# Kernel optimization log

Hardware: AMD Instinct MI355X
Metric: run time of the kernel (lower is better)

Reference implementation:

```python
import jax, jax.numpy as jnp
import numpy as np

N, E, F, L, G, T = 50000, 800000, 128, 3, 256, 10


def _lin_init(key, shape, fan_in):
    s = 1.0 / np.sqrt(fan_in)
    return jax.random.uniform(key, shape, jnp.float32, -s, s)


def setup_inputs() -> dict:
    key = jax.random.key(0)
    ks = jax.random.split(key, 10)
    x = jax.random.normal(ks[0], (N, F), jnp.float32)
    edge_index = jax.random.randint(ks[1], (2, E), 0, N, jnp.int64)
    batch = jnp.sort(jax.random.randint(ks[2], (N,), 0, G, jnp.int64))
    Wl = _lin_init(ks[3], (L, F, F), F)   # lin_l weight per layer
    bl = _lin_init(ks[4], (L, F), F)      # lin_l bias per layer
    Wr = _lin_init(ks[5], (L, F, F), F)   # lin_r weight per layer (no bias)
    W1 = _lin_init(ks[6], (F, L * F), L * F)
    b1 = _lin_init(ks[7], (F,), L * F)
    W2 = _lin_init(ks[8], (T, F), F)
    b2 = _lin_init(ks[9], (T,), F)
    return {"x": x, "edge_index": edge_index, "batch": batch, "Wl": Wl,
            "bl": bl, "Wr": Wr, "W1": W1, "b1": b1, "W2": W2, "b2": b2}


def reference(x, edge_index, batch, Wl, bl, Wr, W1, b1, W2, b2):
    src, dst = edge_index[0], edge_index[1]
    n = x.shape[0]
    # in-degree for mean aggregation (zero-degree nodes -> 0, like scatter_mean)
    deg = jax.ops.segment_sum(jnp.ones_like(src, dtype=x.dtype), dst, num_segments=n)
    inv_deg = jnp.where(deg > 0, 1.0 / deg, 0.0)[:, None]
    h = x
    feats = []
    for i in range(L):
        # SAGEConv (aggr='mean'): out = lin_l(mean_j x_j) + lin_r(x_i)
        agg = jax.ops.segment_sum(h[src], dst, num_segments=n) * inv_deg
        h = agg @ Wl[i].T + bl[i] + h @ Wr[i].T
        feats.append(h)
    hc = jnp.concatenate(feats, axis=1)            # [N, L*F]
    pooled = jax.ops.segment_max(hc, batch, num_segments=G)  # global_max_pool
    z = jax.nn.relu(pooled @ W1.T + b1)
    return z @ W2.T + b2                            # [G, T]
```

## Files before the change

### kernel.cpp

```cpp
#include <hip/hip_runtime.h>
#include <math.h>


typedef __attribute__((ext_vector_type(8))) short short8v;
typedef __attribute__((ext_vector_type(4))) float f32x4;

__device__ __forceinline__ unsigned short bf_hi_bits(float f) {
    union { float f; unsigned u; } c; c.f = f;
    return (unsigned short)(c.u >> 16);
}
__device__ __forceinline__ float bf_to_f(unsigned short h) {
    union { unsigned u; float f; } c; c.u = ((unsigned)h) << 16;
    return c.f;
}
__device__ __forceinline__ unsigned short f2bf_rne(float f) {
    union { float f; unsigned u; } c; c.f = f;
    unsigned u = c.u;
    u += 0x7FFF + ((u >> 16) & 1);
    return (unsigned short)(u >> 16);
}

__global__ void zero_ints(int* __restrict__ p, int n) {
    int i = blockIdx.x * 256 + threadIdx.x;
    if (i < n) p[i] = 0;
}

__global__ void count_deg(const int* __restrict__ dst, int* __restrict__ deg, int E) {
    int e = blockIdx.x * 256 + threadIdx.x;
    if (e < E) atomicAdd(&deg[dst[e]], 1);
}

__global__ __launch_bounds__(256) void block_reduce_deg(const int* __restrict__ deg,
                                                        int* __restrict__ bsum,
                                                        float* __restrict__ inv_deg, int n) {
    __shared__ int s[256];
    int t = threadIdx.x;
    int i = blockIdx.x * 256 + t;
    int d = 0;
    if (i < n) {
        d = deg[i];
        inv_deg[i] = d > 0 ? 1.0f / (float)d : 0.0f;
    }
    s[t] = d;
    __syncthreads();
#pragma unroll
    for (int off = 128; off > 0; off >>= 1) {
        if (t < off) s[t] += s[t + off];
        __syncthreads();
    }
    if (t == 0) bsum[blockIdx.x] = s[0];
}

__global__ __launch_bounds__(256) void scan_bsums(const int* __restrict__ bsum,
                                                  int* __restrict__ boff,
                                                  int* __restrict__ row_ptr, int nb, int n) {
    __shared__ int s[256];
    int t = threadIdx.x;
    int v = (t < nb) ? bsum[t] : 0;
    s[t] = v;
    __syncthreads();
#pragma unroll
    for (int off = 1; off < 256; off <<= 1) {
        int u = (t >= off) ? s[t - off] : 0;
        __syncthreads();
        s[t] += u;
        __syncthreads();
    }
    if (t < nb) boff[t] = s[t] - v;
    if (t == 255) row_ptr[n] = s[255];
}

__global__ __launch_bounds__(256) void scan_fill(const int* __restrict__ deg,
                                                 const int* __restrict__ boff,
                                                 int* __restrict__ row_ptr,
                                                 int* __restrict__ fill_pos, int n) {
    __shared__ int s[256];
    int t = threadIdx.x;
    int i = blockIdx.x * 256 + t;
    int v = (i < n) ? deg[i] : 0;
    s[t] = v;
    __syncthreads();
#pragma unroll
    for (int off = 1; off < 256; off <<= 1) {
        int u = (t >= off) ? s[t - off] : 0;
        __syncthreads();
        s[t] += u;
        __syncthreads();
    }
    if (i < n) {
        int ex = boff[blockIdx.x] + s[t] - v;
        row_ptr[i] = ex;
        fill_pos[i] = ex;
    }
}

__global__ void fill_csr(const int* __restrict__ src, const int* __restrict__ dst,
                         int* __restrict__ fill_pos, int* __restrict__ csr_src, int E) {
    int e = blockIdx.x * 256 + threadIdx.x;
    if (e < E) {
        int d = dst[e];
        int pos = atomicAdd(&fill_pos[d], 1);
        csr_src[pos] = src[e];
    }
}

__global__ void f32_to_bf16(const float* __restrict__ in, unsigned short* __restrict__ out,
                            int n4) {
    int i = blockIdx.x * 256 + threadIdx.x;
    if (i < n4) {
        float4 v = *(const float4*)(in + (size_t)i * 4);
        ushort4 o = {f2bf_rne(v.x), f2bf_rne(v.y), f2bf_rne(v.z), f2bf_rne(v.w)};
        *(ushort4*)(out + (size_t)i * 4) = o;
    }
}

__global__ __launch_bounds__(256) void aggregate_bf(const unsigned short* __restrict__ hb,
                                                    const int* __restrict__ row_ptr,
                                                    const int* __restrict__ csr_src,
                                                    const float* __restrict__ inv_deg,
                                                    float* __restrict__ agg, int n) {
    int node = blockIdx.x * 4 + (threadIdx.x >> 6);
    if (node >= n) return;
    int lane = threadIdx.x & 63;
    int half = lane >> 5;
    int li = lane & 31;
    int j0 = row_ptr[node], j1 = row_ptr[node + 1];
    float a0 = 0.f, a1 = 0.f, a2 = 0.f, a3 = 0.f;
    float b0 = 0.f, b1 = 0.f, b2 = 0.f, b3 = 0.f;
    int j = j0 + half;
    for (; j + 2 < j1; j += 4) {
        int s0 = csr_src[j];
        int s1 = csr_src[j + 2];
        ushort4 v0 = *(const ushort4*)(hb + (size_t)s0 * 128 + li * 4);
        ushort4 v1 = *(const ushort4*)(hb + (size_t)s1 * 128 + li * 4);
        a0 += bf_to_f(v0.x); a1 += bf_to_f(v0.y); a2 += bf_to_f(v0.z); a3 += bf_to_f(v0.w);
        b0 += bf_to_f(v1.x); b1 += bf_to_f(v1.y); b2 += bf_to_f(v1.z); b3 += bf_to_f(v1.w);
    }
    if (j < j1) {
        int s0 = csr_src[j];
        ushort4 v0 = *(const ushort4*)(hb + (size_t)s0 * 128 + li * 4);
        a0 += bf_to_f(v0.x); a1 += bf_to_f(v0.y); a2 += bf_to_f(v0.z); a3 += bf_to_f(v0.w);
    }
    float ax = a0 + b0, ay = a1 + b1, az = a2 + b2, aw = a3 + b3;
    ax += __shfl_xor(ax, 32);
    ay += __shfl_xor(ay, 32);
    az += __shfl_xor(az, 32);
    aw += __shfl_xor(aw, 32);
    if (half == 0) {
        float w = inv_deg[node];
        float4 o = {ax * w, ay * w, az * w, aw * w};
        *(float4*)(agg + (size_t)node * 128 + li * 4) = o;
    }
}

__global__ void prep_wext(const float* __restrict__ Wl, const float* __restrict__ Wr,
                          unsigned short* __restrict__ wext) {
    int idx = blockIdx.x * 256 + threadIdx.x;
    if (idx >= 36864) return;
    int layer = idx / 12288;
    int rem = idx - layer * 12288;
    int s = rem / 2048;
    int rem2 = rem - s * 2048;
    int c = rem2 >> 4;
    int kc = (rem2 & 15) * 8;
    const float* W = (s < 3 ? Wl : Wr) + (size_t)layer * 16384 + c * 128 + kc;
    bool lo = (s % 3) == 1;
    unsigned short* o = wext + (((size_t)layer * 6 + s) * 16384) + c * 128 + kc;
#pragma unroll
    for (int i = 0; i < 8; ++i) {
        float f = W[i];
        unsigned short hb = bf_hi_bits(f);
        if (lo) hb = bf_hi_bits(f - bf_to_f(hb));
        o[i] = hb;
    }
}

__global__ __launch_bounds__(256, 2) void gemm_mfma(const float* __restrict__ A1,
                                                    const float* __restrict__ A2, int stride2,
                                                    const unsigned short* __restrict__ wext,
                                                    const float* __restrict__ bl,
                                                    float* __restrict__ out,
                                                    unsigned short* __restrict__ outb, int n) {
    __shared__ unsigned short Ald[16384];
    __shared__ unsigned short Wld[16384];

    const int tid = threadIdx.x;
    const int row0 = blockIdx.x * 128;
    const int wid = tid >> 6;
    const int lane = tid & 63;
    const int lrow = lane & 15;
    const int lk = lane >> 4;
    const int RowB = (wid >> 1) * 64;
    const int ColB = (wid & 1) * 64;

    const f32x4 zf = {0.f, 0.f, 0.f, 0.f};
    f32x4 acc[4][4];
#pragma unroll
    for (int i = 0; i < 4; ++i)
#pragma unroll
        for (int j = 0; j < 4; ++j) acc[i][j] = zf;

    const int sr = tid >> 1;
    const int sh = tid & 1;
    int grow = row0 + sr;
    if (grow > n - 1) grow = n - 1;
    const float* a1p = A1 + (size_t)grow * 128 + sh * 64;
    const float* a2p = A2 + (size_t)grow * stride2 + sh * 64;
    const int sbyte = sr * 256 + sh * 128;
    const int sswz = (sr & 7) << 4;

    const int needA[6] = {1, 0, 1, 1, 0, 1};
    const int srcA[6] = {0, 0, 0, 1, 1, 1};
    const int loA[6] = {0, 0, 1, 0, 0, 1};

#pragma unroll
    for (int s = 0; s < 6; ++s) {
        const unsigned short* wsrc = wext + s * 16384 + sr * 128 + sh * 64;
#pragma unroll
        for (int i = 0; i < 8; ++i) {
            short8v w = *(const short8v*)(wsrc + i * 8);
            *(short8v*)((char*)Wld + sbyte + ((i * 16) ^ sswz)) = w;
        }
        if (needA[s]) {
            const float* ap = srcA[s] ? a2p : a1p;
            const bool lo = loA[s] != 0;
#pragma unroll
            for (int i = 0; i < 8; ++i) {
                float4 f0 = *(const float4*)(ap + i * 8);
                float4 f1 = *(const float4*)(ap + i * 8 + 4);
                float ff[8] = {f0.x, f0.y, f0.z, f0.w, f1.x, f1.y, f1.z, f1.w};
                short8v v;
#pragma unroll
                for (int j = 0; j < 8; ++j) {
                    unsigned short hb = bf_hi_bits(ff[j]);
                    if (lo) hb = bf_hi_bits(ff[j] - bf_to_f(hb));
                    v[j] = (short)hb;
                }
                *(short8v*)((char*)Ald + sbyte + ((i * 16) ^ sswz)) = v;
            }
        }
        __syncthreads();
#pragma unroll
        for (int ks = 0; ks < 4; ++ks) {
            short8v af[4], bfr[4];
#pragma unroll
            for (int mr = 0; mr < 4; ++mr) {
                int r = RowB + mr * 16 + lrow;
                int byte = (r * 256 + ks * 64 + lk * 16) ^ ((r & 7) << 4);
                af[mr] = *(const short8v*)((const char*)Ald + byte);
            }
#pragma unroll
            for (int nr = 0; nr < 4; ++nr) {
                int c = ColB + nr * 16 + lrow;
                int byte = (c * 256 + ks * 64 + lk * 16) ^ ((c & 7) << 4);
                bfr[nr] = *(const short8v*)((const char*)Wld + byte);
            }
#pragma unroll
            for (int mr = 0; mr < 4; ++mr)
#pragma unroll
                for (int nr = 0; nr < 4; ++nr)
                    acc[mr][nr] = __builtin_amdgcn_mfma_f32_16x16x32_bf16(
                        af[mr], bfr[nr], acc[mr][nr], 0, 0, 0);
        }
        __syncthreads();
    }

#pragma unroll
    for (int nr = 0; nr < 4; ++nr) {
        int col = ColB + nr * 16 + lrow;
        float bias = bl[col];
#pragma unroll
        for (int mr = 0; mr < 4; ++mr) {
            int rbase = row0 + RowB + mr * 16 + lk * 4;
#pragma unroll
            for (int r = 0; r < 4; ++r) {
                int row = rbase + r;
                if (row < n) {
                    float v = acc[mr][nr][r] + bias;
                    out[(size_t)row * 384 + col] = v;
                    if (outb) outb[(size_t)row * 128 + col] = f2bf_rne(v);
                }
            }
        }
    }
}

__global__ void find_starts(const int* __restrict__ batch, int* __restrict__ start, int n, int G) {
    int i = blockIdx.x * 256 + threadIdx.x;
    if (i >= n) return;
    int b = batch[i];
    if (i == 0) {
        for (int g = 0; g <= b; ++g) start[g] = 0;
    } else {
        int pb = batch[i - 1];
        for (int g = pb + 1; g <= b; ++g) start[g] = i;
    }
    if (i == n - 1) {
        for (int g = b + 1; g <= G; ++g) start[g] = n;
    }
}

__global__ __launch_bounds__(384) void pool_max(const float* __restrict__ hc,
                                                const int* __restrict__ start,
                                                float* __restrict__ pooled, int G) {
    int g = blockIdx.x;
    int f = threadIdx.x;
    int s = start[g], e = start[g + 1];
    float m = -INFINITY;
    for (int node = s; node < e; ++node) m = fmaxf(m, hc[(size_t)node * 384 + f]);
    pooled[(size_t)g * 384 + f] = m;
}

__global__ __launch_bounds__(128) void mlp_head(const float* __restrict__ pooled,
                                                const float* __restrict__ W1,
                                                const float* __restrict__ b1,
                                                const float* __restrict__ W2,
                                                const float* __restrict__ b2,
                                                float* __restrict__ out) {
    __shared__ float p[384];
    __shared__ float z[128];
    int g = blockIdx.x, t = threadIdx.x;
    for (int k = t; k < 384; k += 128) p[k] = pooled[(size_t)g * 384 + k];
    __syncthreads();
    float acc = b1[t];
#pragma unroll 4
    for (int k = 0; k < 384; k += 4) {
        float4 w = *(const float4*)(W1 + (size_t)t * 384 + k);
        acc += p[k] * w.x + p[k + 1] * w.y + p[k + 2] * w.z + p[k + 3] * w.w;
    }
    z[t] = fmaxf(acc, 0.f);
    __syncthreads();
    if (t < 10) {
        float a2 = b2[t];
#pragma unroll 8
        for (int k = 0; k < 128; ++k) a2 += z[k] * W2[t * 128 + k];
        out[g * 10 + t] = a2;
    }
}

extern "C" void kernel_launch(void* const* d_in, const int* in_sizes, int n_in,
                              void* d_out, int out_size, void* d_ws, size_t ws_size,
                              hipStream_t stream) {
    const float* x = (const float*)d_in[0];
    const int* edge = (const int*)d_in[1];
    const int* batch = (const int*)d_in[2];
    const float* Wl = (const float*)d_in[3];
    const float* bl = (const float*)d_in[4];
    const float* Wr = (const float*)d_in[5];
    const float* W1 = (const float*)d_in[6];
    const float* b1 = (const float*)d_in[7];
    const float* W2 = (const float*)d_in[8];
    const float* b2 = (const float*)d_in[9];
    float* out = (float*)d_out;

    const int F = 128, G = 256;
    const int N = in_sizes[0] / F;
    const int E = in_sizes[1] / 2;
    const int NB = (N + 255) / 256;

    const int* src = edge;
    const int* dst = edge + E;

    char* p = (char*)d_ws;
    auto alloc = [&](size_t bytes) {
        char* r = p;
        p += (bytes + 15) & ~(size_t)15;
        return r;
    };
    float* hc = (float*)alloc((size_t)N * 384 * 4);
    float* agg = (float*)alloc((size_t)N * 128 * 4);
    float* inv = (float*)alloc((size_t)N * 4);
    float* pooled = (float*)alloc((size_t)G * 384 * 4);
    int* deg = (int*)alloc((size_t)N * 4);
    int* row_ptr = (int*)alloc((size_t)(N + 1) * 4);
    int* fillp = (int*)alloc((size_t)N * 4);
    int* csr = (int*)alloc((size_t)E * 4);
    int* start = (int*)alloc((size_t)(G + 1) * 4);
    unsigned short* wext = (unsigned short*)alloc((size_t)3 * 6 * 16384 * 2);
    int* bsum = (int*)alloc((size_t)NB * 4);
    int* boff = (int*)alloc((size_t)NB * 4);
    unsigned short* hb = (unsigned short*)alloc((size_t)N * 128 * 2);

    zero_ints<<<NB, 256, 0, stream>>>(deg, N);
    count_deg<<<(E + 255) / 256, 256, 0, stream>>>(dst, deg, E);
    block_reduce_deg<<<NB, 256, 0, stream>>>(deg, bsum, inv, N);
    scan_bsums<<<1, 256, 0, stream>>>(bsum, boff, row_ptr, NB, N);
    scan_fill<<<NB, 256, 0, stream>>>(deg, boff, row_ptr, fillp, N);
    fill_csr<<<(E + 255) / 256, 256, 0, stream>>>(src, dst, fillp, csr, E);
    prep_wext<<<144, 256, 0, stream>>>(Wl, Wr, wext);
    f32_to_bf16<<<(N * 32 + 255) / 256, 256, 0, stream>>>(x, hb, N * 32);

    for (int l = 0; l < 3; ++l) {
        const float* hin = (l == 0) ? x : (hc + (size_t)(l - 1) * 128);
        int hstride = (l == 0) ? 128 : 384;
        aggregate_bf<<<(N + 3) / 4, 256, 0, stream>>>(hb, row_ptr, csr, inv, agg, N);
        gemm_mfma<<<(N + 127) / 128, 256, 0, stream>>>(
            agg, hin, hstride, wext + (size_t)l * 6 * 16384, bl + (size_t)l * F,
            hc + (size_t)l * 128, (l < 2) ? hb : (unsigned short*)nullptr, N);
    }

    find_starts<<<NB, 256, 0, stream>>>(batch, start, N, G);
    pool_max<<<G, 384, 0, stream>>>(hc, start, pooled, G);
    mlp_head<<<G, 128, 0, stream>>>(pooled, W1, b1, W2, b2, out);
}
```

Baseline: 500.2 us.

## Store activations as bf16 hi/lo pairs and shrink GEMM row tile to 64

Activations are stored as bf16 hi/lo split pairs instead of fp32. The aggregation kernel now emits the aggregate already split, and the GEMM writes bf16 hi into the concatenated feature buffer plus a lo residual for the next layer. The GEMM loads pre-split bf16 tiles directly, which removes the per-tile fp32-to-bf16 conversion and halves activation traffic. Its row tile shrinks from 128 to 64 with launch bounds raised to 3, giving more blocks and occupancy. The cost is that the pooled features are now bf16-rounded instead of fp32, and each GEMM block has less reuse of the weight tile.

```diff
diff --git a/kernel.cpp b/kernel.cpp
--- a/kernel.cpp
+++ b/kernel.cpp
@@ -104,21 +104,26 @@
     }
 }
 
-__global__ void f32_to_bf16(const float* __restrict__ in, unsigned short* __restrict__ out,
-                            int n4) {
+__global__ void f32_split_bf16(const float* __restrict__ in, unsigned short* __restrict__ hi,
+                               unsigned short* __restrict__ lo, int n4) {
     int i = blockIdx.x * 256 + threadIdx.x;
     if (i < n4) {
         float4 v = *(const float4*)(in + (size_t)i * 4);
-        ushort4 o = {f2bf_rne(v.x), f2bf_rne(v.y), f2bf_rne(v.z), f2bf_rne(v.w)};
-        *(ushort4*)(out + (size_t)i * 4) = o;
+        ushort4 h = {f2bf_rne(v.x), f2bf_rne(v.y), f2bf_rne(v.z), f2bf_rne(v.w)};
+        ushort4 l = {f2bf_rne(v.x - bf_to_f(h.x)), f2bf_rne(v.y - bf_to_f(h.y)),
+                     f2bf_rne(v.z - bf_to_f(h.z)), f2bf_rne(v.w - bf_to_f(h.w))};
+        *(ushort4*)(hi + (size_t)i * 4) = h;
+        *(ushort4*)(lo + (size_t)i * 4) = l;
     }
 }
 
 __global__ __launch_bounds__(256) void aggregate_bf(const unsigned short* __restrict__ hb,
+                                                    int hstride,
                                                     const int* __restrict__ row_ptr,
                                                     const int* __restrict__ csr_src,
                                                     const float* __restrict__ inv_deg,
-                                                    float* __restrict__ agg, int n) {
+                                                    unsigned short* __restrict__ a1hi,
+                                                    unsigned short* __restrict__ a1lo, int n) {
     int node = blockIdx.x * 4 + (threadIdx.x >> 6);
     if (node >= n) return;
     int lane = threadIdx.x & 63;
@@ -131,14 +136,14 @@
     for (; j + 2 < j1; j += 4) {
         int s0 = csr_src[j];
         int s1 = csr_src[j + 2];
-        ushort4 v0 = *(const ushort4*)(hb + (size_t)s0 * 128 + li * 4);
-        ushort4 v1 = *(const ushort4*)(hb + (size_t)s1 * 128 + li * 4);
+        ushort4 v0 = *(const ushort4*)(hb + (size_t)s0 * hstride + li * 4);
+        ushort4 v1 = *(const ushort4*)(hb + (size_t)s1 * hstride + li * 4);
         a0 += bf_to_f(v0.x); a1 += bf_to_f(v0.y); a2 += bf_to_f(v0.z); a3 += bf_to_f(v0.w);
         b0 += bf_to_f(v1.x); b1 += bf_to_f(v1.y); b2 += bf_to_f(v1.z); b3 += bf_to_f(v1.w);
     }
     if (j < j1) {
         int s0 = csr_src[j];
-        ushort4 v0 = *(const ushort4*)(hb + (size_t)s0 * 128 + li * 4);
+        ushort4 v0 = *(const ushort4*)(hb + (size_t)s0 * hstride + li * 4);
         a0 += bf_to_f(v0.x); a1 += bf_to_f(v0.y); a2 += bf_to_f(v0.z); a3 += bf_to_f(v0.w);
     }
     float ax = a0 + b0, ay = a1 + b1, az = a2 + b2, aw = a3 + b3;
@@ -148,8 +153,12 @@
     aw += __shfl_xor(aw, 32);
     if (half == 0) {
         float w = inv_deg[node];
-        float4 o = {ax * w, ay * w, az * w, aw * w};
-        *(float4*)(agg + (size_t)node * 128 + li * 4) = o;
+        float vx = ax * w, vy = ay * w, vz = az * w, vw = aw * w;
+        ushort4 h = {f2bf_rne(vx), f2bf_rne(vy), f2bf_rne(vz), f2bf_rne(vw)};
+        ushort4 l = {f2bf_rne(vx - bf_to_f(h.x)), f2bf_rne(vy - bf_to_f(h.y)),
+                     f2bf_rne(vz - bf_to_f(h.z)), f2bf_rne(vw - bf_to_f(h.w))};
+        *(ushort4*)(a1hi + (size_t)node * 128 + li * 4) = h;
+        *(ushort4*)(a1lo + (size_t)node * 128 + li * 4) = l;
     }
 }
 
@@ -175,82 +184,76 @@
     }
 }
 
-__global__ __launch_bounds__(256, 2) void gemm_mfma(const float* __restrict__ A1,
-                                                    const float* __restrict__ A2, int stride2,
+__global__ __launch_bounds__(256, 3) void gemm_mfma(const unsigned short* __restrict__ a1hi,
+                                                    const unsigned short* __restrict__ a1lo,
+                                                    const unsigned short* __restrict__ a2hi,
+                                                    int stride2,
+                                                    const unsigned short* __restrict__ a2lo,
                                                     const unsigned short* __restrict__ wext,
                                                     const float* __restrict__ bl,
-                                                    float* __restrict__ out,
-                                                    unsigned short* __restrict__ outb, int n) {
-    __shared__ unsigned short Ald[16384];
+                                                    unsigned short* __restrict__ outh,
+                                                    unsigned short* __restrict__ outlo, int n) {
+    __shared__ unsigned short Ald[8192];
     __shared__ unsigned short Wld[16384];
 
     const int tid = threadIdx.x;
-    const int row0 = blockIdx.x * 128;
+    const int row0 = blockIdx.x * 64;
     const int wid = tid >> 6;
     const int lane = tid & 63;
     const int lrow = lane & 15;
     const int lk = lane >> 4;
-    const int RowB = (wid >> 1) * 64;
-    const int ColB = (wid & 1) * 64;
+    const int ColB = wid * 32;
 
     const f32x4 zf = {0.f, 0.f, 0.f, 0.f};
-    f32x4 acc[4][4];
+    f32x4 acc[4][2];
 #pragma unroll
     for (int i = 0; i < 4; ++i)
 #pragma unroll
-        for (int j = 0; j < 4; ++j) acc[i][j] = zf;
-
-    const int sr = tid >> 1;
+        for (int j = 0; j < 2; ++j) acc[i][j] = zf;
+
+    const int sr_a = tid >> 2;
+    const int qa = tid & 3;
+    int growA = row0 + sr_a;
+    if (growA > n - 1) growA = n - 1;
+    const unsigned short* pa1hi = a1hi + (size_t)growA * 128 + qa * 32;
+    const unsigned short* pa1lo = a1lo + (size_t)growA * 128 + qa * 32;
+    const unsigned short* pa2hi = a2hi + (size_t)growA * stride2 + qa * 32;
+    const unsigned short* pa2lo = a2lo + (size_t)growA * 128 + qa * 32;
+    const int aswz = (sr_a & 7) << 4;
+
+    const int sw = tid >> 1;
     const int sh = tid & 1;
-    int grow = row0 + sr;
-    if (grow > n - 1) grow = n - 1;
-    const float* a1p = A1 + (size_t)grow * 128 + sh * 64;
-    const float* a2p = A2 + (size_t)grow * stride2 + sh * 64;
-    const int sbyte = sr * 256 + sh * 128;
-    const int sswz = (sr & 7) << 4;
-
-    const int needA[6] = {1, 0, 1, 1, 0, 1};
-    const int srcA[6] = {0, 0, 0, 1, 1, 1};
-    const int loA[6] = {0, 0, 1, 0, 0, 1};
+    const int wswz = (sw & 7) << 4;
+
+    const unsigned short* asrc[6] = {pa1hi, nullptr, pa1lo, pa2hi, nullptr, pa2lo};
 
 #pragma unroll
     for (int s = 0; s < 6; ++s) {
-        const unsigned short* wsrc = wext + s * 16384 + sr * 128 + sh * 64;
+        const unsigned short* wsrc = wext + s * 16384 + sw * 128 + sh * 64;
 #pragma unroll
         for (int i = 0; i < 8; ++i) {
             short8v w = *(const short8v*)(wsrc + i * 8);
-            *(short8v*)((char*)Wld + sbyte + ((i * 16) ^ sswz)) = w;
+            *(short8v*)((char*)Wld + ((sw * 256 + sh * 128 + i * 16) ^ wswz)) = w;
         }
-        if (needA[s]) {
-            const float* ap = srcA[s] ? a2p : a1p;
-            const bool lo = loA[s] != 0;
-#pragma unroll
-            for (int i = 0; i < 8; ++i) {
-                float4 f0 = *(const float4*)(ap + i * 8);
-                float4 f1 = *(const float4*)(ap + i * 8 + 4);
-                float ff[8] = {f0.x, f0.y, f0.z, f0.w, f1.x, f1.y, f1.z, f1.w};
-                short8v v;
-#pragma unroll
-                for (int j = 0; j < 8; ++j) {
-                    unsigned short hb = bf_hi_bits(ff[j]);
-                    if (lo) hb = bf_hi_bits(ff[j] - bf_to_f(hb));
-                    v[j] = (short)hb;
-                }
-                *(short8v*)((char*)Ald + sbyte + ((i * 16) ^ sswz)) = v;
+        if (asrc[s]) {
+#pragma unroll
+            for (int i = 0; i < 4; ++i) {
+                short8v v = *(const short8v*)(asrc[s] + i * 8);
+                *(short8v*)((char*)Ald + ((sr_a * 256 + qa * 64 + i * 16) ^ aswz)) = v;
             }
         }
         __syncthreads();
 #pragma unroll
         for (int ks = 0; ks < 4; ++ks) {
-            short8v af[4], bfr[4];
+            short8v af[4], bfr[2];
 #pragma unroll
             for (int mr = 0; mr < 4; ++mr) {
-                int r = RowB + mr * 16 + lrow;
+                int r = mr * 16 + lrow;
                 int byte = (r * 256 + ks * 64 + lk * 16) ^ ((r & 7) << 4);
                 af[mr] = *(const short8v*)((const char*)Ald + byte);
             }
 #pragma unroll
-            for (int nr = 0; nr < 4; ++nr) {
+            for (int nr = 0; nr < 2; ++nr) {
                 int c = ColB + nr * 16 + lrow;
                 int byte = (c * 256 + ks * 64 + lk * 16) ^ ((c & 7) << 4);
                 bfr[nr] = *(const short8v*)((const char*)Wld + byte);
@@ -258,7 +261,7 @@
 #pragma unroll
             for (int mr = 0; mr < 4; ++mr)
 #pragma unroll
-                for (int nr = 0; nr < 4; ++nr)
+                for (int nr = 0; nr < 2; ++nr)
                     acc[mr][nr] = __builtin_amdgcn_mfma_f32_16x16x32_bf16(
                         af[mr], bfr[nr], acc[mr][nr], 0, 0, 0);
         }
@@ -266,19 +269,20 @@
     }
 
 #pragma unroll
-    for (int nr = 0; nr < 4; ++nr) {
+    for (int nr = 0; nr < 2; ++nr) {
         int col = ColB + nr * 16 + lrow;
         float bias = bl[col];
 #pragma unroll
         for (int mr = 0; mr < 4; ++mr) {
-            int rbase = row0 + RowB + mr * 16 + lk * 4;
+            int rbase = row0 + mr * 16 + lk * 4;
 #pragma unroll
             for (int r = 0; r < 4; ++r) {
                 int row = rbase + r;
                 if (row < n) {
                     float v = acc[mr][nr][r] + bias;
-                    out[(size_t)row * 384 + col] = v;
-                    if (outb) outb[(size_t)row * 128 + col] = f2bf_rne(v);
+                    unsigned short hv = f2bf_rne(v);
+                    outh[(size_t)row * 384 + col] = hv;
+                    if (outlo) outlo[(size_t)row * 128 + col] = f2bf_rne(v - bf_to_f(hv));
                 }
             }
         }
@@ -300,14 +304,14 @@
     }
 }
 
-__global__ __launch_bounds__(384) void pool_max(const float* __restrict__ hc,
+__global__ __launch_bounds__(384) void pool_max(const unsigned short* __restrict__ hcb,
                                                 const int* __restrict__ start,
                                                 float* __restrict__ pooled, int G) {
     int g = blockIdx.x;
     int f = threadIdx.x;
     int s = start[g], e = start[g + 1];
     float m = -INFINITY;
-    for (int node = s; node < e; ++node) m = fmaxf(m, hc[(size_t)node * 384 + f]);
+    for (int node = s; node < e; ++node) m = fmaxf(m, bf_to_f(hcb[(size_t)node * 384 + f]));
     pooled[(size_t)g * 384 + f] = m;
 }
 
@@ -367,8 +371,12 @@
         p += (bytes + 15) & ~(size_t)15;
         return r;
     };
-    float* hc = (float*)alloc((size_t)N * 384 * 4);
-    float* agg = (float*)alloc((size_t)N * 128 * 4);
+    unsigned short* hcb = (unsigned short*)alloc((size_t)N * 384 * 2);
+    unsigned short* a1hi = (unsigned short*)alloc((size_t)N * 128 * 2);
+    unsigned short* a1lo = (unsigned short*)alloc((size_t)N * 128 * 2);
+    unsigned short* xhi = (unsigned short*)alloc((size_t)N * 128 * 2);
+    unsigned short* xlo = (unsigned short*)alloc((size_t)N * 128 * 2);
+    unsigned short* a2lo = (unsigned short*)alloc((size_t)N * 128 * 2);
     float* inv = (float*)alloc((size_t)N * 4);
     float* pooled = (float*)alloc((size_t)G * 384 * 4);
     int* deg = (int*)alloc((size_t)N * 4);
@@ -379,7 +387,6 @@
     unsigned short* wext = (unsigned short*)alloc((size_t)3 * 6 * 16384 * 2);
     int* bsum = (int*)alloc((size_t)NB * 4);
     int* boff = (int*)alloc((size_t)NB * 4);
-    unsigned short* hb = (unsigned short*)alloc((size_t)N * 128 * 2);
 
     zero_ints<<<NB, 256, 0, stream>>>(deg, N);
     count_deg<<<(E + 255) / 256, 256, 0, stream>>>(dst, deg, E);
@@ -388,18 +395,20 @@
     scan_fill<<<NB, 256, 0, stream>>>(deg, boff, row_ptr, fillp, N);
     fill_csr<<<(E + 255) / 256, 256, 0, stream>>>(src, dst, fillp, csr, E);
     prep_wext<<<144, 256, 0, stream>>>(Wl, Wr, wext);
-    f32_to_bf16<<<(N * 32 + 255) / 256, 256, 0, stream>>>(x, hb, N * 32);
+    f32_split_bf16<<<(N * 32 + 255) / 256, 256, 0, stream>>>(x, xhi, xlo, N * 32);
 
     for (int l = 0; l < 3; ++l) {
-        const float* hin = (l == 0) ? x : (hc + (size_t)(l - 1) * 128);
-        int hstride = (l == 0) ? 128 : 384;
-        aggregate_bf<<<(N + 3) / 4, 256, 0, stream>>>(hb, row_ptr, csr, inv, agg, N);
-        gemm_mfma<<<(N + 127) / 128, 256, 0, stream>>>(
-            agg, hin, hstride, wext + (size_t)l * 6 * 16384, bl + (size_t)l * F,
-            hc + (size_t)l * 128, (l < 2) ? hb : (unsigned short*)nullptr, N);
+        const unsigned short* ghi = (l == 0) ? xhi : (hcb + (size_t)(l - 1) * 128);
+        int gstride = (l == 0) ? 128 : 384;
+        const unsigned short* glo = (l == 0) ? xlo : a2lo;
+        aggregate_bf<<<(N + 3) / 4, 256, 0, stream>>>(ghi, gstride, row_ptr, csr, inv,
+                                                      a1hi, a1lo, N);
+        gemm_mfma<<<(N + 63) / 64, 256, 0, stream>>>(
+            a1hi, a1lo, ghi, gstride, glo, wext + (size_t)l * 6 * 16384, bl + (size_t)l * F,
+            hcb + (size_t)l * 128, (l < 2) ? a2lo : (unsigned short*)nullptr, N);
     }
 
     find_starts<<<NB, 256, 0, stream>>>(batch, start, N, G);
-    pool_max<<<G, 384, 0, stream>>>(hc, start, pooled, G);
+    pool_max<<<G, 384, 0, stream>>>(hcb, start, pooled, G);
     mlp_head<<<G, 128, 0, stream>>>(pooled, W1, b1, W2, b2, out);
 }
```

Result: faster. 480.5 us (-3.9%).
